# Kernel tuning notes

Hardware: AMD Instinct MI355X
Metric: run time of the kernel (lower is better)

## Reference

```python
import jax, jax.numpy as jnp
import numpy as np

EMPHASIS_FACTOR = 1.5

def setup_inputs() -> dict:
    key = jax.random.key(0)
    k1, k2 = jax.random.split(key)
    B, T, F = 32, 4096, 256
    x = jax.random.normal(k1, (B, T, F), dtype=jnp.float32)
    W = jax.random.normal(k2, (F, 1), dtype=jnp.float32) * (1.0 / np.sqrt(F))
    b = jnp.zeros((1,), dtype=jnp.float32)
    return {"x": x, "W": W, "b": b}

def reference(x, W, b):
    # x: [B, T, F], W: [F, 1], b: [1]
    B, T, F = x.shape
    e = jnp.tanh(x @ W + b)                 # [B, T, 1]
    a = jax.nn.softmax(e, axis=1)           # softmax over time
    a_flat = a[..., 0]                      # [B, T]
    k = max(1, int(T * 0.1))
    _, top_idx = jax.lax.top_k(a_flat, k)   # [B, k]
    # scatter True at top-k positions (instead of O(T*k) broadcast compare)
    mask = jnp.zeros((B, T), dtype=bool).at[jnp.arange(B)[:, None], top_idx].set(True)
    a_emph = jnp.where(mask[..., None], a * EMPHASIS_FACTOR, a)  # [B, T, 1]
    return jnp.sum(x * a_emph, axis=1, keepdims=True)            # [B, 1, F]
```

## Files before the change

### kernel.cpp

```cpp
#include <hip/hip_runtime.h>
#include <math.h>

#define BB 32
#define TT 4096
#define FF 256
#define CH 64
#define NC (TT / CH)
#define K_TOP 409
#define EMPH_HALF 0.5f
#define NSEG 32
#define SEGT (TT / NSEG)
#define CPS (NC / NSEG)

__device__ __forceinline__ unsigned flip_key(float v) {
    unsigned u = __float_as_uint(v);
    return (u & 0x80000000u) ? ~u : (u | 0x80000000u);
}
__device__ __forceinline__ float fast_tanh(float z) {
    z = fminf(fmaxf(z, -15.f), 15.f);
    const float t = __expf(2.f * z);
    return (t - 1.f) * __builtin_amdgcn_rcpf(t + 1.f);
}

__global__ __launch_bounds__(256) void fused_pass1(const float* __restrict__ x,
                                                   const float* __restrict__ W,
                                                   const float* __restrict__ bias,
                                                   float* __restrict__ e,
                                                   float* __restrict__ P,
                                                   float* __restrict__ cm,
                                                   float* __restrict__ cs,
                                                   float* __restrict__ out) {
    const int b = blockIdx.x / NC;
    const int c = blockIdx.x % NC;
    const int tid = threadIdx.x;
    const int wv = tid >> 6, ln = tid & 63;

    if (c == 0) out[b * FF + tid] = 0.f;

    const float* xc = x + ((size_t)b * TT + (size_t)c * CH) * FF;
    const float4 wvec = ((const float4*)W)[ln];
    const float  bb   = bias[0];

    float4 acc = make_float4(0.f, 0.f, 0.f, 0.f);
    float  m = -1e30f, ssum = 0.f;

    #pragma unroll
    for (int s0 = 0; s0 < CH; s0 += 16) {
        const int r0 = s0 + wv * 4;
        float4 xr[4];
        #pragma unroll
        for (int i = 0; i < 4; i++)
            xr[i] = ((const float4*)(xc + (size_t)(r0 + i) * FF))[ln];

        float dv[4];
        #pragma unroll
        for (int i = 0; i < 4; i++)
            dv[i] = xr[i].x * wvec.x + xr[i].y * wvec.y +
                    xr[i].z * wvec.z + xr[i].w * wvec.w;
        #pragma unroll
        for (int i = 0; i < 4; i++) {
            float d = dv[i];
            #pragma unroll
            for (int off = 32; off; off >>= 1) d += __shfl_xor(d, off);
            dv[i] = fast_tanh(d + bb);
        }
        if (ln == 0)
            *(float4*)(e + (size_t)b * TT + c * CH + r0) =
                make_float4(dv[0], dv[1], dv[2], dv[3]);

        float lm = m;
        #pragma unroll
        for (int i = 0; i < 4; i++) lm = fmaxf(lm, dv[i]);
        const float alpha = __expf(m - lm);
        acc.x *= alpha; acc.y *= alpha; acc.z *= alpha; acc.w *= alpha;
        ssum *= alpha;
        #pragma unroll
        for (int i = 0; i < 4; i++) {
            const float wgt = __expf(dv[i] - lm);
            ssum += wgt;
            acc.x += wgt * xr[i].x; acc.y += wgt * xr[i].y;
            acc.z += wgt * xr[i].z; acc.w += wgt * xr[i].w;
        }
        m = lm;
    }

    __shared__ float4 part4[4][64];
    __shared__ float sm[4], ss4[4];
    part4[wv][ln] = acc;
    if (ln == 0) { sm[wv] = m; ss4[wv] = ssum; }
    __syncthreads();

    const float m0 = sm[0], m1 = sm[1], m2 = sm[2], m3 = sm[3];
    const float mc = fmaxf(fmaxf(m0, m1), fmaxf(m2, m3));
    const float s0s = __expf(m0 - mc), s1s = __expf(m1 - mc);
    const float s2s = __expf(m2 - mc), s3s = __expf(m3 - mc);
    const float* pf = (const float*)part4;
    const float p = pf[tid] * s0s + pf[256 + tid] * s1s +
                    pf[512 + tid] * s2s + pf[768 + tid] * s3s;
    P[((size_t)b * NC + c) * FF + tid] = p;
    if (tid == 0) {
        cm[b * NC + c] = mc;
        cs[b * NC + c] = ss4[0] * s0s + ss4[1] * s1s + ss4[2] * s2s + ss4[3] * s3s;
    }
}

__global__ __launch_bounds__(256) void select_kernel(const float* __restrict__ e,
                                                     const float* __restrict__ cm,
                                                     const float* __restrict__ cs,
                                                     float* __restrict__ stats) {
    const int b = blockIdx.x;
    const int tid = threadIdx.x;
    const int wv = tid >> 6, ln = tid & 63;

    float g = 0.f, zz = 0.f;
    if (tid < 64) {
        const float mm = cm[b * NC + tid];
        const float ss = cs[b * NC + tid];
        g = mm;
        #pragma unroll
        for (int off = 32; off; off >>= 1) g = fmaxf(g, __shfl_xor(g, off));
        zz = ss * __expf(mm - g);
        #pragma unroll
        for (int off = 32; off; off >>= 1) zz += __shfl_xor(zz, off);
    }

    const float4* eb4 = (const float4*)(e + (size_t)b * TT);
    unsigned key[16];
    #pragma unroll
    for (int j = 0; j < 4; j++) {
        const float4 v = eb4[tid + 256 * j];
        key[4 * j + 0] = flip_key(v.x);
        key[4 * j + 1] = flip_key(v.y);
        key[4 * j + 2] = flip_key(v.z);
        key[4 * j + 3] = flip_key(v.w);
    }

    __shared__ int sc[2][4];
    unsigned prefix = 0u, mask = 0u;
    int kk = K_TOP;
    int pb = 0;
    for (int bit = 31; bit >= 0; bit--) {
        const unsigned bm = 1u << bit;
        const unsigned m2 = mask | bm;
        const unsigned want = prefix | bm;
        int cnt = 0;
        #pragma unroll
        for (int j = 0; j < 16; j++)
            cnt += (int)__popcll(__ballot((key[j] & m2) == want));
        if (ln == 0) sc[pb][wv] = cnt;
        __syncthreads();
        const int tot = sc[pb][0] + sc[pb][1] + sc[pb][2] + sc[pb][3];
        pb ^= 1;
        if (tot >= kk) {
            prefix = want;
            if (tot == kk) break;
        } else {
            kk -= tot;
        }
        mask = m2;
    }

    if (tid == 0) {
        stats[3 * b + 0] = g;
        stats[3 * b + 1] = zz;
        stats[3 * b + 2] = __uint_as_float(prefix);
    }
}

__global__ __launch_bounds__(256) void combine_kernel(const float* __restrict__ x,
                                                      const float* __restrict__ e,
                                                      const float* __restrict__ P,
                                                      const float* __restrict__ cm,
                                                      const float* __restrict__ stats,
                                                      float* __restrict__ out) {
    const int b = blockIdx.x / NSEG;
    const int s = blockIdx.x % NSEG;
    const int tid = threadIdx.x;

    const float gmax = stats[3 * b + 0];
    const float Z    = stats[3 * b + 1];
    const unsigned Kkey = __float_as_uint(stats[3 * b + 2]);

    float acc = 0.f;
    #pragma unroll
    for (int c = 0; c < CPS; c++) {
        const int cc = s * CPS + c;
        const float sc2 = __expf(cm[b * NC + cc] - gmax);
        acc += P[((size_t)b * NC + cc) * FF + tid] * sc2;
    }

    __shared__ int scount;
    __shared__ int slist[SEGT];
    __shared__ float sval[SEGT];
    if (tid == 0) scount = 0;
    __syncthreads();

    if (tid < SEGT) {
        const int t = s * SEGT + tid;
        const float ev = e[(size_t)b * TT + t];
        if (flip_key(ev) >= Kkey) {
            const int i = atomicAdd(&scount, 1);
            slist[i] = t;
            sval[i] = EMPH_HALF * __expf(ev - gmax);
        }
    }
    __syncthreads();

    const int n = scount;
    const float* xb = x + (size_t)b * TT * FF;
    int i = 0;
    for (; i + 4 <= n; i += 4) {
        const float* p0 = xb + (size_t)slist[i + 0] * FF;
        const float* p1 = xb + (size_t)slist[i + 1] * FF;
        const float* p2 = xb + (size_t)slist[i + 2] * FF;
        const float* p3 = xb + (size_t)slist[i + 3] * FF;
        const float w0 = sval[i + 0], w1 = sval[i + 1];
        const float w2 = sval[i + 2], w3 = sval[i + 3];
        acc += w0 * p0[tid] + w1 * p1[tid] + w2 * p2[tid] + w3 * p3[tid];
    }
    for (; i < n; i++)
        acc += sval[i] * xb[(size_t)slist[i] * FF + tid];

    atomicAdd(&out[b * FF + tid], acc * (1.f / Z));
}

extern "C" void kernel_launch(void* const* d_in, const int* in_sizes, int n_in,
                              void* d_out, int out_size, void* d_ws, size_t ws_size,
                              hipStream_t stream) {
    const float* x    = (const float*)d_in[0];
    const float* W    = (const float*)d_in[1];
    const float* bias = (const float*)d_in[2];
    float* out = (float*)d_out;

    float* e     = (float*)d_ws;
    float* P     = e + (size_t)BB * TT;
    float* cm    = P + (size_t)BB * NC * FF;
    float* cs    = cm + BB * NC;
    float* stats = cs + BB * NC;

    fused_pass1<<<BB * NC, 256, 0, stream>>>(x, W, bias, e, P, cm, cs, out);
    select_kernel<<<BB, 256, 0, stream>>>(e, cm, cs, stats);
    combine_kernel<<<BB * NSEG, 256, 0, stream>>>(x, e, P, cm, stats, out);
}
```

Before: 207.3 us.

## Merge top-k select and combine kernels into one launch with flag handoff

Fuses the select and combine kernels into a single tail kernel. The first BB blocks each run the radix select on one wave with 64 keys per lane, which removes the per-bit __syncthreads, and add an early exit once the remaining candidates equal k. They publish the threshold key through a global flag that the combine blocks spin on. The combine blocks recompute the softmax max and normalizer themselves and do the P rescaling and e loads before waiting, so that work overlaps the select. This saves a kernel launch and boundary, but it relies on the selector blocks being scheduled ahead of the spinning blocks (blocks with lower indices), and it uses many registers per lane.

```diff
diff --git a/kernel.cpp b/kernel.cpp
--- a/kernel.cpp
+++ b/kernel.cpp
@@ -29,13 +29,17 @@
                                                    float* __restrict__ P,
                                                    float* __restrict__ cm,
                                                    float* __restrict__ cs,
+                                                   unsigned* __restrict__ kflag,
                                                    float* __restrict__ out) {
     const int b = blockIdx.x / NC;
     const int c = blockIdx.x % NC;
     const int tid = threadIdx.x;
     const int wv = tid >> 6, ln = tid & 63;
 
-    if (c == 0) out[b * FF + tid] = 0.f;
+    if (c == 0) {
+        out[b * FF + tid] = 0.f;
+        if (tid == 0) kflag[b] = 0u;
+    }
 
     const float* xc = x + ((size_t)b * TT + (size_t)c * CH) * FF;
     const float4 wvec = ((const float4*)W)[ln];
@@ -104,105 +108,105 @@
     }
 }
 
-__global__ __launch_bounds__(256) void select_kernel(const float* __restrict__ e,
-                                                     const float* __restrict__ cm,
-                                                     const float* __restrict__ cs,
-                                                     float* __restrict__ stats) {
-    const int b = blockIdx.x;
-    const int tid = threadIdx.x;
-    const int wv = tid >> 6, ln = tid & 63;
-
-    float g = 0.f, zz = 0.f;
-    if (tid < 64) {
-        const float mm = cm[b * NC + tid];
-        const float ss = cs[b * NC + tid];
-        g = mm;
-        #pragma unroll
-        for (int off = 32; off; off >>= 1) g = fmaxf(g, __shfl_xor(g, off));
-        zz = ss * __expf(mm - g);
-        #pragma unroll
-        for (int off = 32; off; off >>= 1) zz += __shfl_xor(zz, off);
-    }
-
-    const float4* eb4 = (const float4*)(e + (size_t)b * TT);
-    unsigned key[16];
-    #pragma unroll
-    for (int j = 0; j < 4; j++) {
-        const float4 v = eb4[tid + 256 * j];
-        key[4 * j + 0] = flip_key(v.x);
-        key[4 * j + 1] = flip_key(v.y);
-        key[4 * j + 2] = flip_key(v.z);
-        key[4 * j + 3] = flip_key(v.w);
-    }
-
-    __shared__ int sc[2][4];
-    unsigned prefix = 0u, mask = 0u;
-    int kk = K_TOP;
-    int pb = 0;
-    for (int bit = 31; bit >= 0; bit--) {
-        const unsigned bm = 1u << bit;
-        const unsigned m2 = mask | bm;
-        const unsigned want = prefix | bm;
-        int cnt = 0;
-        #pragma unroll
-        for (int j = 0; j < 16; j++)
-            cnt += (int)__popcll(__ballot((key[j] & m2) == want));
-        if (ln == 0) sc[pb][wv] = cnt;
-        __syncthreads();
-        const int tot = sc[pb][0] + sc[pb][1] + sc[pb][2] + sc[pb][3];
-        pb ^= 1;
-        if (tot >= kk) {
-            prefix = want;
-            if (tot == kk) break;
-        } else {
-            kk -= tot;
-        }
-        mask = m2;
-    }
-
-    if (tid == 0) {
-        stats[3 * b + 0] = g;
-        stats[3 * b + 1] = zz;
-        stats[3 * b + 2] = __uint_as_float(prefix);
-    }
-}
-
-__global__ __launch_bounds__(256) void combine_kernel(const float* __restrict__ x,
+__global__ __launch_bounds__(256, 5) void tail_kernel(const float* __restrict__ x,
                                                       const float* __restrict__ e,
                                                       const float* __restrict__ P,
                                                       const float* __restrict__ cm,
-                                                      const float* __restrict__ stats,
+                                                      const float* __restrict__ cs,
+                                                      unsigned* __restrict__ kflag,
                                                       float* __restrict__ out) {
-    const int b = blockIdx.x / NSEG;
-    const int s = blockIdx.x % NSEG;
     const int tid = threadIdx.x;
 
-    const float gmax = stats[3 * b + 0];
-    const float Z    = stats[3 * b + 1];
-    const unsigned Kkey = __float_as_uint(stats[3 * b + 2]);
+    if (blockIdx.x < BB) {
+        if (tid >= 64) return;
+        const int b = blockIdx.x;
+        const float4* eb4 = (const float4*)(e + (size_t)b * TT);
+        unsigned key[64];
+        #pragma unroll
+        for (int j = 0; j < 16; j++) {
+            const float4 v = eb4[j * 64 + tid];
+            key[4 * j + 0] = flip_key(v.x);
+            key[4 * j + 1] = flip_key(v.y);
+            key[4 * j + 2] = flip_key(v.z);
+            key[4 * j + 3] = flip_key(v.w);
+        }
+        unsigned prefix = 0u, mask = 0u;
+        int kk = K_TOP, ncand = TT;
+        for (int bit = 31; bit >= 0; bit--) {
+            const unsigned bm = 1u << bit;
+            const unsigned m2 = mask | bm;
+            const unsigned want = prefix | bm;
+            int cnt = 0;
+            #pragma unroll
+            for (int j = 0; j < 64; j++)
+                cnt += (int)__popcll(__ballot((key[j] & m2) == want));
+            if (cnt >= kk) {
+                prefix = want;
+                if (cnt == kk) break;
+                ncand = cnt;
+            } else {
+                kk -= cnt;
+                ncand -= cnt;
+                if (ncand == kk) break;
+            }
+            mask = m2;
+        }
+        if (tid == 0)
+            __hip_atomic_store(kflag + b, prefix,
+                               __ATOMIC_RELAXED, __HIP_MEMORY_SCOPE_AGENT);
+        return;
+    }
+
+    const int cb = blockIdx.x - BB;
+    const int b = cb / NSEG;
+    const int s = cb % NSEG;
+    const int ln = tid & 63;
+
+    const float cmv = cm[b * NC + ln];
+    const float csv = cs[b * NC + ln];
+    float g = cmv;
+    #pragma unroll
+    for (int off = 32; off; off >>= 1) g = fmaxf(g, __shfl_xor(g, off));
+    float zz = csv * __expf(cmv - g);
+    #pragma unroll
+    for (int off = 32; off; off >>= 1) zz += __shfl_xor(zz, off);
 
     float acc = 0.f;
     #pragma unroll
     for (int c = 0; c < CPS; c++) {
         const int cc = s * CPS + c;
-        const float sc2 = __expf(cm[b * NC + cc] - gmax);
-        acc += P[((size_t)b * NC + cc) * FF + tid] * sc2;
-    }
-
+        const float mcc = __shfl(cmv, cc);
+        acc += P[((size_t)b * NC + cc) * FF + tid] * __expf(mcc - g);
+    }
+
+    int t = 0; unsigned ky = 0u; float pv = 0.f;
+    if (tid < SEGT) {
+        t = s * SEGT + tid;
+        const float ev = e[(size_t)b * TT + t];
+        ky = flip_key(ev);
+        pv = EMPH_HALF * __expf(ev - g);
+    }
+
+    __shared__ unsigned skey;
     __shared__ int scount;
     __shared__ int slist[SEGT];
     __shared__ float sval[SEGT];
-    if (tid == 0) scount = 0;
+    if (tid == 0) {
+        scount = 0;
+        unsigned k;
+        do {
+            k = __hip_atomic_load(kflag + b,
+                                  __ATOMIC_RELAXED, __HIP_MEMORY_SCOPE_AGENT);
+        } while (k == 0u);
+        skey = k;
+    }
     __syncthreads();
-
-    if (tid < SEGT) {
-        const int t = s * SEGT + tid;
-        const float ev = e[(size_t)b * TT + t];
-        if (flip_key(ev) >= Kkey) {
-            const int i = atomicAdd(&scount, 1);
-            slist[i] = t;
-            sval[i] = EMPH_HALF * __expf(ev - gmax);
-        }
+    const unsigned Kkey = skey;
+
+    if (tid < SEGT && ky >= Kkey) {
+        const int i = atomicAdd(&scount, 1);
+        slist[i] = t;
+        sval[i] = pv;
     }
     __syncthreads();
 
@@ -221,7 +225,7 @@
     for (; i < n; i++)
         acc += sval[i] * xb[(size_t)slist[i] * FF + tid];
 
-    atomicAdd(&out[b * FF + tid], acc * (1.f / Z));
+    atomicAdd(&out[b * FF + tid], acc * (1.f / zz));
 }
 
 extern "C" void kernel_launch(void* const* d_in, const int* in_sizes, int n_in,
@@ -236,9 +240,8 @@
     float* P     = e + (size_t)BB * TT;
     float* cm    = P + (size_t)BB * NC * FF;
     float* cs    = cm + BB * NC;
-    float* stats = cs + BB * NC;
-
-    fused_pass1<<<BB * NC, 256, 0, stream>>>(x, W, bias, e, P, cm, cs, out);
-    select_kernel<<<BB, 256, 0, stream>>>(e, cm, cs, stats);
-    combine_kernel<<<BB * NSEG, 256, 0, stream>>>(x, e, P, cm, stats, out);
-}
+    unsigned* kf = (unsigned*)(cs + BB * NC);
+
+    fused_pass1<<<BB * NC, 256, 0, stream>>>(x, W, bias, e, P, cm, cs, kf, out);
+    tail_kernel<<<BB + BB * NSEG, 256, 0, stream>>>(x, e, P, cm, cs, kf, out);
+}
```

New measurement: 225.9 us. 1.09x slower.

## Fuse top-k threshold selection into combine kernel, removing separate select launch

Applied to the files above, without the earlier changes.

The select kernel is merged into the combine kernel. Each of the 32 segment blocks per batch now recomputes the softmax max/normaliser and the radix-select threshold over all 4096 scores itself, so the stats buffer round-trip and one kernel launch go away. The radix loop also gains an early exit once the remaining candidates exactly equal the count still needed. The cost is 32x redundant selection work per batch, about 32 barrier-synchronised iterations in every combine block, in exchange for fewer launches and more parallelism than the previous 32-block select kernel.

```diff
diff --git a/kernel.cpp b/kernel.cpp
--- a/kernel.cpp
+++ b/kernel.cpp
@@ -104,25 +104,25 @@
     }
 }
 
-__global__ __launch_bounds__(256) void select_kernel(const float* __restrict__ e,
-                                                     const float* __restrict__ cm,
-                                                     const float* __restrict__ cs,
-                                                     float* __restrict__ stats) {
-    const int b = blockIdx.x;
+__global__ __launch_bounds__(256) void combine_kernel(const float* __restrict__ x,
+                                                      const float* __restrict__ e,
+                                                      const float* __restrict__ P,
+                                                      const float* __restrict__ cm,
+                                                      const float* __restrict__ cs,
+                                                      float* __restrict__ out) {
+    const int b = blockIdx.x / NSEG;
+    const int s = blockIdx.x % NSEG;
     const int tid = threadIdx.x;
     const int wv = tid >> 6, ln = tid & 63;
 
-    float g = 0.f, zz = 0.f;
-    if (tid < 64) {
-        const float mm = cm[b * NC + tid];
-        const float ss = cs[b * NC + tid];
-        g = mm;
-        #pragma unroll
-        for (int off = 32; off; off >>= 1) g = fmaxf(g, __shfl_xor(g, off));
-        zz = ss * __expf(mm - g);
-        #pragma unroll
-        for (int off = 32; off; off >>= 1) zz += __shfl_xor(zz, off);
-    }
+    const float cmv = cm[b * NC + ln];
+    const float csv = cs[b * NC + ln];
+    float g = cmv;
+    #pragma unroll
+    for (int off = 32; off; off >>= 1) g = fmaxf(g, __shfl_xor(g, off));
+    float zz = csv * __expf(cmv - g);
+    #pragma unroll
+    for (int off = 32; off; off >>= 1) zz += __shfl_xor(zz, off);
 
     const float4* eb4 = (const float4*)(e + (size_t)b * TT);
     unsigned key[16];
@@ -135,9 +135,30 @@
         key[4 * j + 3] = flip_key(v.w);
     }
 
+    float acc = 0.f;
+    #pragma unroll
+    for (int c = 0; c < CPS; c++) {
+        const int cc = s * CPS + c;
+        const float mcc = __shfl(cmv, cc);
+        acc += P[((size_t)b * NC + cc) * FF + tid] * __expf(mcc - g);
+    }
+
+    int t = 0; unsigned ky = 0u; float pv = 0.f;
+    if (tid < SEGT) {
+        t = s * SEGT + tid;
+        const float ev = e[(size_t)b * TT + t];
+        ky = flip_key(ev);
+        pv = EMPH_HALF * __expf(ev - g);
+    }
+
     __shared__ int sc[2][4];
+    __shared__ int scount;
+    __shared__ int slist[SEGT];
+    __shared__ float sval[SEGT];
+    if (tid == 0) scount = 0;
+
     unsigned prefix = 0u, mask = 0u;
-    int kk = K_TOP;
+    int kk = K_TOP, ncand = TT;
     int pb = 0;
     for (int bit = 31; bit >= 0; bit--) {
         const unsigned bm = 1u << bit;
@@ -154,55 +175,20 @@
         if (tot >= kk) {
             prefix = want;
             if (tot == kk) break;
+            ncand = tot;
         } else {
             kk -= tot;
+            ncand -= tot;
+            if (ncand == kk) break;
         }
         mask = m2;
     }
-
-    if (tid == 0) {
-        stats[3 * b + 0] = g;
-        stats[3 * b + 1] = zz;
-        stats[3 * b + 2] = __uint_as_float(prefix);
-    }
-}
-
-__global__ __launch_bounds__(256) void combine_kernel(const float* __restrict__ x,
-                                                      const float* __restrict__ e,
-                                                      const float* __restrict__ P,
-                                                      const float* __restrict__ cm,
-                                                      const float* __restrict__ stats,
-                                                      float* __restrict__ out) {
-    const int b = blockIdx.x / NSEG;
-    const int s = blockIdx.x % NSEG;
-    const int tid = threadIdx.x;
-
-    const float gmax = stats[3 * b + 0];
-    const float Z    = stats[3 * b + 1];
-    const unsigned Kkey = __float_as_uint(stats[3 * b + 2]);
-
-    float acc = 0.f;
-    #pragma unroll
-    for (int c = 0; c < CPS; c++) {
-        const int cc = s * CPS + c;
-        const float sc2 = __expf(cm[b * NC + cc] - gmax);
-        acc += P[((size_t)b * NC + cc) * FF + tid] * sc2;
-    }
-
-    __shared__ int scount;
-    __shared__ int slist[SEGT];
-    __shared__ float sval[SEGT];
-    if (tid == 0) scount = 0;
-    __syncthreads();
-
-    if (tid < SEGT) {
-        const int t = s * SEGT + tid;
-        const float ev = e[(size_t)b * TT + t];
-        if (flip_key(ev) >= Kkey) {
-            const int i = atomicAdd(&scount, 1);
-            slist[i] = t;
-            sval[i] = EMPH_HALF * __expf(ev - gmax);
-        }
+    const unsigned Kkey = prefix;
+
+    if (tid < SEGT && ky >= Kkey) {
+        const int i = atomicAdd(&scount, 1);
+        slist[i] = t;
+        sval[i] = pv;
     }
     __syncthreads();
 
@@ -221,7 +207,7 @@
     for (; i < n; i++)
         acc += sval[i] * xb[(size_t)slist[i] * FF + tid];
 
-    atomicAdd(&out[b * FF + tid], acc * (1.f / Z));
+    atomicAdd(&out[b * FF + tid], acc * (1.f / zz));
 }
 
 extern "C" void kernel_launch(void* const* d_in, const int* in_sizes, int n_in,
@@ -236,9 +222,7 @@
     float* P     = e + (size_t)BB * TT;
     float* cm    = P + (size_t)BB * NC * FF;
     float* cs    = cm + BB * NC;
-    float* stats = cs + BB * NC;
 
     fused_pass1<<<BB * NC, 256, 0, stream>>>(x, W, bias, e, P, cm, cs, out);
-    select_kernel<<<BB, 256, 0, stream>>>(e, cm, cs, stats);
-    combine_kernel<<<BB * NSEG, 256, 0, stream>>>(x, e, P, cm, stats, out);
-}
+    combine_kernel<<<BB * NSEG, 256, 0, stream>>>(x, e, P, cm, cs, out);
+}
```

Measured after the change: 210.4 us. About the same (+1.5%).
